# Performance work log

Measured on AMD Instinct MI355X. Metric: run time of the kernel, lower is better.

The kernel has to match this reference:

```python
import jax, jax.numpy as jnp
import numpy as np
import math

B, C, H, W = 16, 256, 48, 48
CK = C // 8


def setup_inputs() -> dict:
    key = jax.random.key(0)
    ks = jax.random.split(key, 8)
    s = 0.05
    return {
        "x": jax.random.normal(ks[0], (B, C, H, W), dtype=jnp.float32),
        "Wq": jax.random.normal(ks[1], (CK, C), dtype=jnp.float32) * s,
        "bq": jax.random.normal(ks[2], (CK,), dtype=jnp.float32) * s,
        "Wk": jax.random.normal(ks[3], (CK, C), dtype=jnp.float32) * s,
        "bk": jax.random.normal(ks[4], (CK,), dtype=jnp.float32) * s,
        "Wv": jax.random.normal(ks[5], (C, C), dtype=jnp.float32) * s,
        "bv": jax.random.normal(ks[6], (C,), dtype=jnp.float32) * s,
        "gamma": jax.random.normal(ks[7], (1,), dtype=jnp.float32) * 0.1,
    }


def reference(x, Wq, bq, Wk, bk, Wv, bv, gamma):
    b, c, h, w = x.shape
    n = h * w
    xf = x.reshape(b, c, n)  # [B, C, N] (1x1 conv == channel matmul)
    q = jnp.einsum("oc,bcn->bno", Wq, xf) + bq  # [B, N, C/8]
    k = jnp.einsum("oc,bcn->bon", Wk, xf) + bk[None, :, None]  # [B, C/8, N]
    v = jnp.einsum("oc,bcn->bon", Wv, xf) + bv[None, :, None]  # [B, C, N]
    # NOTE: original scales by sqrt(C) (d_k = C), not sqrt(C//8)
    energy = jnp.einsum("bnd,bdm->bnm", q, k) / math.sqrt(c)  # [B, N, N]
    attn = jax.nn.softmax(energy, axis=-1)
    # out[b,c,i] = sum_j v[b,c,j] * attn[b,i,j]
    out = jnp.einsum("bcj,bij->bci", v, attn).reshape(b, c, h, w)
    return gamma[0] * out + x
```

## Files before the change

### kernel.cpp

```cpp
#include <hip/hip_runtime.h>
#include <hip/hip_bf16.h>

#define Bn  16
#define Cn  256
#define CKn 32
#define Nn  2304

typedef __attribute__((ext_vector_type(16))) float f32x16;
typedef __attribute__((ext_vector_type(8)))  short bf16x8;
typedef __attribute__((ext_vector_type(4)))  int   i32x4;

union FragU { unsigned u[4]; bf16x8 v; };
union KU    { i32x4 i; bf16x8 v; };

__device__ __forceinline__ unsigned pk(float lo, float hi){
  unsigned a = (unsigned)__bfloat16_as_ushort(__float2bfloat16(lo));
  unsigned b = (unsigned)__bfloat16_as_ushort(__float2bfloat16(hi));
  return a | (b << 16);
}

__device__ __forceinline__ void halfswap(unsigned A, unsigned Bv, int ,
                                         unsigned &w0, unsigned &w2){
  asm("v_permlane32_swap_b32 %0, %1" : "+v"(A), "+v"(Bv));
  w0 = A; w2 = Bv;
}

__device__ __forceinline__ void conv_store(const f32x16& a, int h, int l,
                                           __hip_bfloat16* dst0, size_t stride){
  unsigned Wp[8];
  #pragma unroll
  for (int q = 0; q < 8; ++q) Wp[q] = pk(a[2*q], a[2*q+1]);
  #pragma unroll
  for (int k2 = 0; k2 < 2; ++k2){
    FragU u;
    halfswap(Wp[4*k2+0], Wp[4*k2+2], h, u.u[0], u.u[2]);
    halfswap(Wp[4*k2+1], Wp[4*k2+3], h, u.u[1], u.u[3]);
    *(bf16x8*)(dst0 + k2*stride + l*8) = u.v;
  }
}

__device__ __forceinline__ void gld16(const void* g, void* l){
  __builtin_amdgcn_global_load_lds(
      (__attribute__((address_space(1))) void*)const_cast<void*>(g),
      (__attribute__((address_space(3))) void*)l, 16, 0, 0);
}

__global__ __launch_bounds__(64) void wfrag_kernel(
    const float* __restrict__ Wq, const float* __restrict__ bq,
    const float* __restrict__ Wk, const float* __restrict__ bk,
    const float* __restrict__ Wv, const float* __restrict__ bv,
    __hip_bfloat16* __restrict__ Wf){
  const int kt = blockIdx.x / 10, tile = blockIdx.x % 10;
  const int l = threadIdx.x, lo = l & 31, h = l >> 5;
  __hip_bfloat16* dst = Wf + (size_t)(kt*10 + tile)*512 + l*8;
  if (kt < 16){
    const float* Wp; int row;
    if (tile < 8)       { Wp = Wv; row = tile*32 + lo; }
    else if (tile == 8) { Wp = Wq; row = lo; }
    else                { Wp = Wk; row = lo; }
    #pragma unroll
    for (int e = 0; e < 8; ++e)
      dst[e] = __float2bfloat16(Wp[(size_t)row*Cn + kt*16 + 8*h + e]);
  } else {
    const float* bp = tile < 8 ? bv : (tile == 8 ? bq : bk);
    int row = tile < 8 ? tile*32 + lo : lo;
    #pragma unroll
    for (int e = 0; e < 8; ++e)
      dst[e] = __float2bfloat16((h == 0 && e == 0) ? bp[row] : 0.f);
  }
}

__global__ __launch_bounds__(256) void proj_kernel(
    const float* __restrict__ x, const __hip_bfloat16* __restrict__ Wf,
    __hip_bfloat16* __restrict__ Qf, __hip_bfloat16* __restrict__ Kf,
    __hip_bfloat16* __restrict__ Vf){
  const int u = blockIdx.x*4 + (threadIdx.x >> 6);
  const int b = u / 72, n32 = u % 72;
  const int l = threadIdx.x & 63, lo = l & 31, h = l >> 5;
  const int n0 = n32*32;

  f32x16 acc[10];
  #pragma unroll
  for (int t = 0; t < 10; ++t)
    #pragma unroll
    for (int r = 0; r < 16; ++r) acc[t][r] = 0.f;

  const float* xb = x + (size_t)b*Cn*Nn + n0 + lo;

  #pragma unroll 1
  for (int kt = 0; kt < 16; ++kt){
    FragU xf;
    float v[8];
    #pragma unroll
    for (int e = 0; e < 8; ++e) v[e] = xb[(size_t)(kt*16 + 8*h + e)*Nn];
    #pragma unroll
    for (int q = 0; q < 4; ++q) xf.u[q] = pk(v[2*q], v[2*q+1]);
    const __hip_bfloat16* wfp = Wf + (size_t)(kt*10)*512 + l*8;
    #pragma unroll
    for (int t = 0; t < 10; ++t){
      bf16x8 wf = *(const bf16x8*)(wfp + t*512);
      if (t < 8) acc[t] = __builtin_amdgcn_mfma_f32_32x32x16_bf16(xf.v, wf, acc[t], 0,0,0);
      else       acc[t] = __builtin_amdgcn_mfma_f32_32x32x16_bf16(wf, xf.v, acc[t], 0,0,0);
    }
  }
  {
    FragU xf;
    xf.u[0] = h ? 0u : 0x00003f80u;
    xf.u[1] = xf.u[2] = xf.u[3] = 0u;
    const __hip_bfloat16* wfp = Wf + (size_t)(16*10)*512 + l*8;
    #pragma unroll
    for (int t = 0; t < 10; ++t){
      bf16x8 wf = *(const bf16x8*)(wfp + t*512);
      if (t < 8) acc[t] = __builtin_amdgcn_mfma_f32_32x32x16_bf16(xf.v, wf, acc[t], 0,0,0);
      else       acc[t] = __builtin_amdgcn_mfma_f32_32x32x16_bf16(wf, xf.v, acc[t], 0,0,0);
    }
  }

  #pragma unroll
  for (int r = 0; r < 16; ++r) acc[8][r] *= 0.09016844f;

  #pragma unroll
  for (int t = 0; t < 8; ++t)
    conv_store(acc[t], h, l, Vf + (((size_t)b*144 + n32*2)*8 + t)*512, 8*512);
  conv_store(acc[8], h, l, Qf + ((size_t)b*72 + n32)*2*512, 512);
  conv_store(acc[9], h, l, Kf + ((size_t)b*72 + n32)*2*512, 512);
}

__global__ __launch_bounds__(192, 2) void attn_kernel(
    const __hip_bfloat16* __restrict__ Qf, const __hip_bfloat16* __restrict__ Kf,
    const __hip_bfloat16* __restrict__ Vf, const float* __restrict__ x,
    const float* __restrict__ gptr, float* __restrict__ out){
  __shared__ __align__(16) char smem[49152];
  const int xcd = blockIdx.x & 7, seq = blockIdx.x >> 3;
  const int b    = xcd*2 + (seq / 48);
  const int rem  = seq % 48;
  const int q24  = rem >> 1;
  const int ch   = rem & 1;
  const int tid = threadIdx.x;
  const int w = tid >> 6, l = tid & 63, lo = l & 31, h = l >> 5;

  const char* vlane = (const char*)Vf + ((size_t)b*1152 + ch*4)*1024 + (size_t)l*16;
  const char* klane = (const char*)Kf + (size_t)b*147456 + (size_t)l*16;

  auto stageV = [&](int jt, int buf){
    const char* gt = vlane + (size_t)jt*32768;
    #pragma unroll
    for (int r = 0; r < 5; ++r){
      const int f = r*3 + w;
      gld16(gt + (f >> 2)*8192 + (f & 3)*1024, smem + buf*16384 + f*1024);
    }
    gld16(gt + 3*8192 + 3*1024, smem + buf*16384 + 15*1024);
  };
  auto kload = [&](int jn, KU (&kf)[2][2]){
    const char* ka = klane + (size_t)jn*4096;
    asm volatile("global_load_dwordx4 %0, %1, off"             : "=v"(kf[0][0].i) : "v"(ka) : "memory");
    asm volatile("global_load_dwordx4 %0, %1, off offset:1024" : "=v"(kf[0][1].i) : "v"(ka) : "memory");
    asm volatile("global_load_dwordx4 %0, %1, off offset:2048" : "=v"(kf[1][0].i) : "v"(ka) : "memory");
    asm volatile("global_load_dwordx4 %0, %1, off offset:3072" : "=v"(kf[1][1].i) : "v"(ka) : "memory");
  };

  bf16x8 qf[2];
  #pragma unroll
  for (int kt = 0; kt < 2; ++kt)
    qf[kt] = *(const bf16x8*)(Qf + (((size_t)b*72 + q24*3 + w)*2 + kt)*512 + l*8);

  f32x16 acc4[4];
  #pragma unroll
  for (int c = 0; c < 4; ++c)
    #pragma unroll
    for (int r = 0; r < 16; ++r) acc4[c][r] = 0.f;
  float lsum = 0.f;

  KU kfA[2][2], kfB[2][2];

  kload(0, kfA);
  stageV(0, 0);
  stageV(1, 1);

  auto body = [&](int jt, KU (&cur)[2][2], KU (&nxt)[2][2], int vb){
    asm volatile("s_waitcnt vmcnt(6)" ::: "memory");
    __builtin_amdgcn_s_barrier();
    __builtin_amdgcn_sched_barrier(0);
    int jn = jt + 1; if (jn >= 36) jn -= 36;
    kload(jn, nxt);
    int j2 = jt + 2; if (j2 >= 36) j2 -= 36;
    int sb = vb + 2; if (sb >= 3) sb -= 3;
    stageV(j2, sb);

    f32x16 z;
    #pragma unroll
    for (int r = 0; r < 16; ++r) z[r] = 0.f;
    f32x16 S0 = __builtin_amdgcn_mfma_f32_32x32x16_bf16(cur[0][0].v, qf[0], z, 0,0,0);
    S0 = __builtin_amdgcn_mfma_f32_32x32x16_bf16(cur[0][1].v, qf[1], S0, 0,0,0);
    f32x16 S1 = __builtin_amdgcn_mfma_f32_32x32x16_bf16(cur[1][0].v, qf[0], z, 0,0,0);
    S1 = __builtin_amdgcn_mfma_f32_32x32x16_bf16(cur[1][1].v, qf[1], S1, 0,0,0);

    FragU pf[4];
    float s0 = 0.f, s1 = 0.f, s2 = 0.f, s3 = 0.f;
    {
      unsigned Wp[8];
      #pragma unroll
      for (int q = 0; q < 4; ++q){
        float p0 = __builtin_amdgcn_exp2f(S0[2*q]);
        float p1 = __builtin_amdgcn_exp2f(S0[2*q+1]);
        s0 += p0 + p1; Wp[q] = pk(p0, p1);
      }
      #pragma unroll
      for (int q = 4; q < 8; ++q){
        float p0 = __builtin_amdgcn_exp2f(S0[2*q]);
        float p1 = __builtin_amdgcn_exp2f(S0[2*q+1]);
        s1 += p0 + p1; Wp[q] = pk(p0, p1);
      }
      halfswap(Wp[0], Wp[2], h, pf[0].u[0], pf[0].u[2]);
      halfswap(Wp[1], Wp[3], h, pf[0].u[1], pf[0].u[3]);
      halfswap(Wp[4], Wp[6], h, pf[1].u[0], pf[1].u[2]);
      halfswap(Wp[5], Wp[7], h, pf[1].u[1], pf[1].u[3]);
    }
    {
      unsigned Wp[8];
      #pragma unroll
      for (int q = 0; q < 4; ++q){
        float p0 = __builtin_amdgcn_exp2f(S1[2*q]);
        float p1 = __builtin_amdgcn_exp2f(S1[2*q+1]);
        s2 += p0 + p1; Wp[q] = pk(p0, p1);
      }
      #pragma unroll
      for (int q = 4; q < 8; ++q){
        float p0 = __builtin_amdgcn_exp2f(S1[2*q]);
        float p1 = __builtin_amdgcn_exp2f(S1[2*q+1]);
        s3 += p0 + p1; Wp[q] = pk(p0, p1);
      }
      halfswap(Wp[0], Wp[2], h, pf[2].u[0], pf[2].u[2]);
      halfswap(Wp[1], Wp[3], h, pf[2].u[1], pf[2].u[3]);
      halfswap(Wp[4], Wp[6], h, pf[3].u[0], pf[3].u[2]);
      halfswap(Wp[5], Wp[7], h, pf[3].u[1], pf[3].u[3]);
    }
    lsum += (s0 + s1) + (s2 + s3);

    const char* cbV = smem + vb*16384;
    #pragma unroll
    for (int js = 0; js < 4; ++js){
      #pragma unroll
      for (int c = 0; c < 4; ++c){
        bf16x8 v = *(const bf16x8*)(cbV + (js*4 + c)*1024 + l*16);
        acc4[c] = __builtin_amdgcn_mfma_f32_32x32x16_bf16(v, pf[js].v, acc4[c], 0,0,0);
      }
    }
  };

  #pragma unroll 1
  for (int jt = 0; jt < 36; jt += 6){
    body(jt+0, kfA, kfB, 0);
    body(jt+1, kfB, kfA, 1);
    body(jt+2, kfA, kfB, 2);
    body(jt+3, kfB, kfA, 0);
    body(jt+4, kfA, kfB, 1);
    body(jt+5, kfB, kfA, 2);
  }

  lsum += __shfl_xor(lsum, 32);
  const float sc = gptr[0] / lsum;
  const int ibase = q24*96 + w*32;
  #pragma unroll
  for (int c = 0; c < 4; ++c){
    #pragma unroll
    for (int r = 0; r < 16; ++r){
      const int cg = ch*128 + c*32 + (r & 3) + 8*(r >> 2) + 4*h;
      const size_t idx = ((size_t)b*Cn + cg)*Nn + ibase + lo;
      out[idx] = acc4[c][r]*sc + x[idx];
    }
  }
}

extern "C" void kernel_launch(void* const* d_in, const int* in_sizes, int n_in,
                              void* d_out, int out_size, void* d_ws, size_t ws_size,
                              hipStream_t stream) {
  const float* x     = (const float*)d_in[0];
  const float* Wq    = (const float*)d_in[1];
  const float* bq    = (const float*)d_in[2];
  const float* Wk    = (const float*)d_in[3];
  const float* bk    = (const float*)d_in[4];
  const float* Wv    = (const float*)d_in[5];
  const float* bv    = (const float*)d_in[6];
  const float* gamma = (const float*)d_in[7];
  float* out = (float*)d_out;

  __hip_bfloat16* Qf = (__hip_bfloat16*)d_ws;
  __hip_bfloat16* Kf = Qf + (size_t)Bn*72*2*512;
  __hip_bfloat16* Vf = Kf + (size_t)Bn*72*2*512;
  __hip_bfloat16* Wf = Vf + (size_t)Bn*144*8*512;

  wfrag_kernel<<<dim3(170), dim3(64), 0, stream>>>(Wq, bq, Wk, bk, Wv, bv, Wf);
  proj_kernel<<<dim3(288), dim3(256), 0, stream>>>(x, Wf, Qf, Kf, Vf);
  attn_kernel<<<dim3(768), dim3(192), 0, stream>>>(Qf, Kf, Vf, x, gamma, out);
}
```

Before: 104.3 us.

## Software-pipeline QK softmax with PV across iterations; split proj blocks to single waves

The attention loop is restructured so the QK MFMA and softmax for tile j+1 are issued alongside the PV MFMAs for tile j. K fragments are now prefetched two tiles ahead, with a prologue and epilogue added. This aims to hide exp and permute latency behind matrix work, at the cost of more registers for the double-buffered probability fragments. Separately, the projection kernel is launched as 1152 one-wave blocks instead of 288 four-wave blocks, which changes scheduling granularity.

```diff
diff --git a/kernel.cpp b/kernel.cpp
--- a/kernel.cpp
+++ b/kernel.cpp
@@ -70,11 +70,11 @@
   }
 }
 
-__global__ __launch_bounds__(256) void proj_kernel(
+__global__ __launch_bounds__(64) void proj_kernel(
     const float* __restrict__ x, const __hip_bfloat16* __restrict__ Wf,
     __hip_bfloat16* __restrict__ Qf, __hip_bfloat16* __restrict__ Kf,
     __hip_bfloat16* __restrict__ Vf){
-  const int u = blockIdx.x*4 + (threadIdx.x >> 6);
+  const int u = blockIdx.x;
   const int b = u / 72, n32 = u % 72;
   const int l = threadIdx.x & 63, lo = l & 31, h = l >> 5;
   const int n0 = n32*32;
@@ -171,31 +171,16 @@
     for (int r = 0; r < 16; ++r) acc4[c][r] = 0.f;
   float lsum = 0.f;
 
-  KU kfA[2][2], kfB[2][2];
-
-  kload(0, kfA);
-  stageV(0, 0);
-  stageV(1, 1);
-
-  auto body = [&](int jt, KU (&cur)[2][2], KU (&nxt)[2][2], int vb){
-    asm volatile("s_waitcnt vmcnt(6)" ::: "memory");
-    __builtin_amdgcn_s_barrier();
-    __builtin_amdgcn_sched_barrier(0);
-    int jn = jt + 1; if (jn >= 36) jn -= 36;
-    kload(jn, nxt);
-    int j2 = jt + 2; if (j2 >= 36) j2 -= 36;
-    int sb = vb + 2; if (sb >= 3) sb -= 3;
-    stageV(j2, sb);
-
+  auto qk = [&](KU (&kf)[2][2], f32x16& S0, f32x16& S1){
     f32x16 z;
     #pragma unroll
     for (int r = 0; r < 16; ++r) z[r] = 0.f;
-    f32x16 S0 = __builtin_amdgcn_mfma_f32_32x32x16_bf16(cur[0][0].v, qf[0], z, 0,0,0);
-    S0 = __builtin_amdgcn_mfma_f32_32x32x16_bf16(cur[0][1].v, qf[1], S0, 0,0,0);
-    f32x16 S1 = __builtin_amdgcn_mfma_f32_32x32x16_bf16(cur[1][0].v, qf[0], z, 0,0,0);
-    S1 = __builtin_amdgcn_mfma_f32_32x32x16_bf16(cur[1][1].v, qf[1], S1, 0,0,0);
-
-    FragU pf[4];
+    S0 = __builtin_amdgcn_mfma_f32_32x32x16_bf16(kf[0][0].v, qf[0], z, 0,0,0);
+    S0 = __builtin_amdgcn_mfma_f32_32x32x16_bf16(kf[0][1].v, qf[1], S0, 0,0,0);
+    S1 = __builtin_amdgcn_mfma_f32_32x32x16_bf16(kf[1][0].v, qf[0], z, 0,0,0);
+    S1 = __builtin_amdgcn_mfma_f32_32x32x16_bf16(kf[1][1].v, qf[1], S1, 0,0,0);
+  };
+  auto softmax = [&](const f32x16& S0, const f32x16& S1, FragU (&pf)[4]){
     float s0 = 0.f, s1 = 0.f, s2 = 0.f, s3 = 0.f;
     {
       unsigned Wp[8];
@@ -236,7 +221,8 @@
       halfswap(Wp[5], Wp[7], h, pf[3].u[1], pf[3].u[3]);
     }
     lsum += (s0 + s1) + (s2 + s3);
-
+  };
+  auto pv = [&](FragU (&pf)[4], int vb){
     const char* cbV = smem + vb*16384;
     #pragma unroll
     for (int js = 0; js < 4; ++js){
@@ -248,15 +234,55 @@
     }
   };
 
+  KU kfA[2][2], kfB[2][2];
+  FragU pfA[4], pfB[4];
+
+  kload(0, kfA);
+  stageV(0, 0);
+  kload(1, kfB);
+  stageV(1, 1);
+  asm volatile("s_waitcnt vmcnt(16)" ::: "memory");
+  __builtin_amdgcn_sched_barrier(0);
+  {
+    f32x16 S0, S1;
+    qk(kfA, S0, S1);
+    softmax(S0, S1, pfA);
+  }
+
+  auto body = [&](int jt, KU (&kq)[2][2], KU (&kl)[2][2],
+                  FragU (&pfu)[4], FragU (&pfw)[4], int vb){
+    asm volatile("s_waitcnt vmcnt(6)" ::: "memory");
+    __builtin_amdgcn_s_barrier();
+    __builtin_amdgcn_sched_barrier(0);
+    int j2 = jt + 2; if (j2 >= 36) j2 -= 36;
+    kload(j2, kl);
+    int sb = vb + 2; if (sb >= 3) sb -= 3;
+    stageV(j2, sb);
+    f32x16 S0, S1;
+    qk(kq, S0, S1);
+    pv(pfu, vb);
+    softmax(S0, S1, pfw);
+  };
+
   #pragma unroll 1
-  for (int jt = 0; jt < 36; jt += 6){
-    body(jt+0, kfA, kfB, 0);
-    body(jt+1, kfB, kfA, 1);
-    body(jt+2, kfA, kfB, 2);
-    body(jt+3, kfB, kfA, 0);
-    body(jt+4, kfA, kfB, 1);
-    body(jt+5, kfB, kfA, 2);
-  }
+  for (int jt = 0; jt < 30; jt += 6){
+    body(jt+0, kfB, kfA, pfA, pfB, 0);
+    body(jt+1, kfA, kfB, pfB, pfA, 1);
+    body(jt+2, kfB, kfA, pfA, pfB, 2);
+    body(jt+3, kfA, kfB, pfB, pfA, 0);
+    body(jt+4, kfB, kfA, pfA, pfB, 1);
+    body(jt+5, kfA, kfB, pfB, pfA, 2);
+  }
+  body(30, kfB, kfA, pfA, pfB, 0);
+  body(31, kfA, kfB, pfB, pfA, 1);
+  body(32, kfB, kfA, pfA, pfB, 2);
+  body(33, kfA, kfB, pfB, pfA, 0);
+  body(34, kfB, kfA, pfA, pfB, 1);
+
+  asm volatile("s_waitcnt vmcnt(10)" ::: "memory");
+  __builtin_amdgcn_s_barrier();
+  __builtin_amdgcn_sched_barrier(0);
+  pv(pfB, 2);
 
   lsum += __shfl_xor(lsum, 32);
   const float sc = gptr[0] / lsum;
@@ -291,6 +317,6 @@
   __hip_bfloat16* Wf = Vf + (size_t)Bn*144*8*512;
 
   wfrag_kernel<<<dim3(170), dim3(64), 0, stream>>>(Wq, bq, Wk, bk, Wv, bv, Wf);
-  proj_kernel<<<dim3(288), dim3(256), 0, stream>>>(x, Wf, Qf, Kf, Vf);
+  proj_kernel<<<dim3(1152), dim3(64), 0, stream>>>(x, Wf, Qf, Kf, Vf);
   attn_kernel<<<dim3(768), dim3(192), 0, stream>>>(Qf, Kf, Vf, x, gamma, out);
 }
```

After: 129.7 us. 24.3% more time.
